# Optimization experiments

Hardware: AMD Instinct MI355X
Metric: run time of the kernel (lower is better)

Reference implementation:

```python
import jax, jax.numpy as jnp
import numpy as np

N, D_IN = 65536, 512
X_DIMS = [512, 2048, 2048, 512]
Y_DIMS = [512, 1024, 512]
T = 2            # n_treatments
OUT_DIM = 1


def setup_inputs() -> dict:
    key = jax.random.key(0)
    ks = iter(jax.random.split(key, 32))
    s = 0.02
    inp = {
        "x": jax.random.normal(next(ks), (N, D_IN), dtype=jnp.float32),
        "treatment": jax.random.randint(next(ks), (N,), 0, T, dtype=jnp.int64),
        # shared trunk MLP (Linear+ReLU after EVERY linear, per original code)
        "Wx0": jax.random.normal(next(ks), (X_DIMS[0], X_DIMS[1]), jnp.float32) * s,
        "bx0": jnp.zeros((X_DIMS[1],), jnp.float32),
        "Wx1": jax.random.normal(next(ks), (X_DIMS[1], X_DIMS[2]), jnp.float32) * s,
        "bx1": jnp.zeros((X_DIMS[2],), jnp.float32),
        "Wx2": jax.random.normal(next(ks), (X_DIMS[2], X_DIMS[3]), jnp.float32) * s,
        "bx2": jnp.zeros((X_DIMS[3],), jnp.float32),
        # per-treatment expert MLPs, stacked on leading T axis
        "Wy0": jax.random.normal(next(ks), (T, Y_DIMS[0], Y_DIMS[1]), jnp.float32) * s,
        "by0": jnp.zeros((T, Y_DIMS[1]), jnp.float32),
        "Wy1": jax.random.normal(next(ks), (T, Y_DIMS[1], Y_DIMS[2]), jnp.float32) * s,
        "by1": jnp.zeros((T, Y_DIMS[2]), jnp.float32),
        # per-treatment output heads
        "Wo": jax.random.normal(next(ks), (T, Y_DIMS[2], OUT_DIM), jnp.float32) * s,
        "bo": jnp.zeros((T, OUT_DIM), jnp.float32),
        # propensity head
        "Wt": jax.random.normal(next(ks), (X_DIMS[3], 1), jnp.float32) * s,
        "bt": jnp.zeros((1,), jnp.float32),
    }
    return inp


def reference(x, treatment, Wx0, bx0, Wx1, bx1, Wx2, bx2,
              Wy0, by0, Wy1, by1, Wo, bo, Wt, bt):
    # shared trunk: ReLU follows every Linear (original MLP applies ReLU after
    # the last layer too, because `i < len(dims)-1` is always true in the loop)
    h = jax.nn.relu(x @ Wx0 + bx0)
    h = jax.nn.relu(h @ Wx1 + bx1)
    x_emb = jax.nn.relu(h @ Wx2 + bx2)            # [N, 512]

    # per-treatment experts computed densely, then gathered by treatment id.
    # This is the dense-equivalent of SplitStreams -> MLP -> GatherStreams:
    # GatherStreams sorts by original row index, so row n of the output is the
    # treatment-`t[n]` head applied to x_emb[n].
    g = jax.nn.relu(jnp.einsum('nd,tdh->nth', x_emb, Wy0) + by0)   # [N,T,1024]
    g = jax.nn.relu(jnp.einsum('nth,thk->ntk', g, Wy1) + by1)      # [N,T,512]
    y_all = jnp.einsum('ntk,tko->nto', g, Wo) + bo                 # [N,T,1]

    t_idx = treatment.astype(jnp.int32).reshape(-1)
    y = jnp.take_along_axis(y_all, t_idx[:, None, None], axis=1)[:, 0, :]  # [N,1]

    # softmax over a size-1 axis -> all ones, but kept faithful to the source
    t_out = jax.nn.softmax(x_emb @ Wt + bt, axis=1)                # [N,1]
    return y, x_emb, t_out
```

## Files before the change

kernel.cpp:

```cpp
#include <hip/hip_runtime.h>
#include <hip/hip_bf16.h>
#include <cstdint>

#define NROWS 65536
#define TTREAT 2

typedef __bf16 bf16x8 __attribute__((ext_vector_type(8)));
typedef float f32x4 __attribute__((ext_vector_type(4)));
typedef unsigned short u16;
typedef u16 u16x8 __attribute__((ext_vector_type(8)));

#define GLOBAL_AS __attribute__((address_space(1)))
#define LDS_AS __attribute__((address_space(3)))

__device__ __forceinline__ int swz_col(int col, int row) {
    return (col & ~63) | (((((col >> 3) & 7) ^ (row & 7)) << 3)) | (col & 7);
}

__device__ __forceinline__ u16 f32_to_bf16_bits(float f) {
    union { float f; uint32_t u; } v; v.f = f;
    uint32_t u = v.u;
    return (u16)((u + 0x7FFFu + ((u >> 16) & 1u)) >> 16);
}

__device__ __forceinline__ float bf16_bits_to_f32(u16 b) {
    union { uint32_t u; float f; } v; v.u = ((uint32_t)b) << 16;
    return v.f;
}

__global__ void cvt_f32_bf16(const float4* __restrict__ src, u16x8* __restrict__ dst, int n8) {
    int i = blockIdx.x * blockDim.x + threadIdx.x;
    if (i >= n8) return;
    float4 a = src[2 * i], b = src[2 * i + 1];
    u16x8 r;
    r[0] = f32_to_bf16_bits(a.x); r[1] = f32_to_bf16_bits(a.y);
    r[2] = f32_to_bf16_bits(a.z); r[3] = f32_to_bf16_bits(a.w);
    r[4] = f32_to_bf16_bits(b.x); r[5] = f32_to_bf16_bits(b.y);
    r[6] = f32_to_bf16_bits(b.z); r[7] = f32_to_bf16_bits(b.w);
    int row = i >> 6;
    int j = (i & ~7) | ((i ^ row) & 7);
    dst[j] = r;
}

__global__ void transpose_w(const float* __restrict__ src, u16* __restrict__ dst, int K, int M) {
    __shared__ float tile[32][33];
    size_t boff = (size_t)blockIdx.z * K * M;
    src += boff; dst += boff;
    int m0 = blockIdx.x * 32, k0 = blockIdx.y * 32;
    int tx = threadIdx.x, ty = threadIdx.y;
#pragma unroll
    for (int i = 0; i < 32; i += 8)
        tile[ty + i][tx] = src[(size_t)(k0 + ty + i) * M + m0 + tx];
    __syncthreads();
#pragma unroll
    for (int i = 0; i < 32; i += 8) {
        int row = m0 + ty + i, col = k0 + tx;
        dst[(size_t)row * K + swz_col(col, row)] = f32_to_bf16_bits(tile[tx][ty + i]);
    }
}

__global__ void zero_cnt(int* cnt) {
    if (threadIdx.x < TTREAT) cnt[threadIdx.x] = 0;
}

__global__ void partition_rows(const int* __restrict__ treat, int* __restrict__ idx, int* __restrict__ cnt) {
    __shared__ int waveCnt1[4];
    __shared__ int blockBase[2];
    const int tid = threadIdx.x;
    const int i = blockIdx.x * 256 + tid;
    const int wave = tid >> 6, lane = tid & 63;
    const int t = treat[i];
    const unsigned long long m1 = __ballot(t == 1);
    const int n1 = __popcll(m1);
    if (lane == 0) waveCnt1[wave] = n1;
    __syncthreads();
    const int w0 = waveCnt1[0], w1 = waveCnt1[1], w2 = waveCnt1[2], w3 = waveCnt1[3];
    const int tot1 = w0 + w1 + w2 + w3;
    if (tid == 0) blockBase[0] = atomicAdd(&cnt[0], 256 - tot1);
    else if (tid == 64) blockBase[1] = atomicAdd(&cnt[1], tot1);
    __syncthreads();
    int waveOff1 = 0;
    if (wave > 0) waveOff1 += w0;
    if (wave > 1) waveOff1 += w1;
    if (wave > 2) waveOff1 += w2;
    const int below1 = (int)__popcll(m1 & ((1ull << lane) - 1ull));
    int pos;
    if (t == 1) pos = blockBase[1] + waveOff1 + below1;
    else        pos = blockBase[0] + (wave * 64 - waveOff1) + (lane - below1);
    idx[t * NROWS + pos] = i;
}

template <bool GATHER, bool WRITE_F32>
__global__ void gemm_bias_relu(const u16* __restrict__ A, const u16* __restrict__ Bt,
                               const float* __restrict__ bias,
                               u16* __restrict__ C, float* __restrict__ C32,
                               const int* __restrict__ idx, const int* __restrict__ cntp,
                               int nrows, int chunkStart, int maxRows, int K, int M) {
    int rows = (cntp ? *cntp : nrows) - chunkStart;
    if (rows > maxRows) rows = maxRows;
    int rowBase = blockIdx.y * 128;
    if (rows <= 0 || rowBase >= rows) return;
    int colBase = blockIdx.x * 128;

    __shared__ __align__(16) u16 As[128 * 64];
    __shared__ __align__(16) u16 Bs[128 * 64];

    const int tid = threadIdx.x;
    const int wave = tid >> 6, lane = tid & 63;
    const int quad = lane >> 4, l16 = lane & 15;
    const int wm = wave >> 1, wn = wave & 1;

    const int r0 = tid >> 3;
    const int kc = (tid & 7) * 8;

    size_t a_off[4], b_off[4];
#pragma unroll
    for (int it = 0; it < 4; ++it) {
        int r = rowBase + r0 + it * 32;
        if (GATHER) {
            int rc = r < rows ? r : (rows - 1);
            int g = idx[rc];
            int kcg = ((((tid & 7) ^ (r & 7) ^ (g & 7)) & 7) * 8);
            a_off[it] = (size_t)g * K + kcg;
        } else {
            a_off[it] = (size_t)r * K + kc;
        }
        int c = colBase + r0 + it * 32;
        b_off[it] = (size_t)c * K + kc;
    }

    f32x4 acc[4][4] = {};

    for (int k0 = 0; k0 < K; k0 += 64) {
        __syncthreads();
#pragma unroll
        for (int it = 0; it < 4; ++it) {
            __builtin_amdgcn_global_load_lds(
                (const GLOBAL_AS void*)(A + a_off[it] + k0),
                (LDS_AS void*)(&As[(it * 256 + wave * 64) * 8]), 16, 0, 0);
            __builtin_amdgcn_global_load_lds(
                (const GLOBAL_AS void*)(Bt + b_off[it] + k0),
                (LDS_AS void*)(&Bs[(it * 256 + wave * 64) * 8]), 16, 0, 0);
        }
        __syncthreads();
#pragma unroll
        for (int kk = 0; kk < 2; ++kk) {
            bf16x8 aF[4], bF[4];
            const int csw = ((kk * 4 + quad) ^ (l16 & 7)) * 8;
#pragma unroll
            for (int mi = 0; mi < 4; ++mi)
                aF[mi] = *(const bf16x8*)&As[(wm * 64 + mi * 16 + l16) * 64 + csw];
#pragma unroll
            for (int ni = 0; ni < 4; ++ni)
                bF[ni] = *(const bf16x8*)&Bs[(wn * 64 + ni * 16 + l16) * 64 + csw];
#pragma unroll
            for (int mi = 0; mi < 4; ++mi)
#pragma unroll
                for (int ni = 0; ni < 4; ++ni)
                    acc[mi][ni] = __builtin_amdgcn_mfma_f32_16x16x32_bf16(
                        aF[mi], bF[ni], acc[mi][ni], 0, 0, 0);
        }
    }

    float bv[4];
#pragma unroll
    for (int ni = 0; ni < 4; ++ni) bv[ni] = bias[colBase + wn * 64 + ni * 16 + l16];

#pragma unroll
    for (int mi = 0; mi < 4; ++mi) {
        int rloc = rowBase + wm * 64 + mi * 16 + quad * 4;
#pragma unroll
        for (int ni = 0; ni < 4; ++ni) {
            int col = colBase + wn * 64 + ni * 16 + l16;
#pragma unroll
            for (int r = 0; r < 4; ++r) {
                int row = rloc + r;
                if (row < rows) {
                    float v = acc[mi][ni][r] + bv[ni];
                    v = v > 0.f ? v : 0.f;
                    C[(size_t)row * M + swz_col(col, row)] = f32_to_bf16_bits(v);
                    if (WRITE_F32) C32[(size_t)row * M + col] = v;
                }
            }
        }
    }
}

__global__ void head_kernel(const u16* __restrict__ g2, const int* __restrict__ idx,
                            const int* __restrict__ cntp, int chunkStart, int maxRows,
                            const float* __restrict__ Wo,
                            const float* __restrict__ bo, float* __restrict__ y) {
    int rows = *cntp - chunkStart;
    if (rows > maxRows) rows = maxRows;
    int wave = threadIdx.x >> 6, lane = threadIdx.x & 63;
    int pos = blockIdx.x * 4 + wave;
    if (pos >= rows) return;
    const u16* grow = g2 + (size_t)pos * 512;
    u16x8 gv = *(const u16x8*)&grow[lane * 8];
    int logical = (lane & ~7) | ((lane ^ pos) & 7);
    const float4* w4 = (const float4*)Wo + logical * 2;
    float4 w0 = w4[0], w1 = w4[1];
    float s = 0.f;
    s += bf16_bits_to_f32(gv[0]) * w0.x + bf16_bits_to_f32(gv[1]) * w0.y;
    s += bf16_bits_to_f32(gv[2]) * w0.z + bf16_bits_to_f32(gv[3]) * w0.w;
    s += bf16_bits_to_f32(gv[4]) * w1.x + bf16_bits_to_f32(gv[5]) * w1.y;
    s += bf16_bits_to_f32(gv[6]) * w1.z + bf16_bits_to_f32(gv[7]) * w1.w;
#pragma unroll
    for (int off = 32; off > 0; off >>= 1) s += __shfl_down(s, off);
    if (lane == 0) y[idx[pos]] = s + bo[0];
}

__global__ void ones_kernel(float* __restrict__ dst, int n) {
    int i = blockIdx.x * 256 + threadIdx.x;
    if (i < n) dst[i] = 1.0f;
}

extern "C" void kernel_launch(void* const* d_in, const int* in_sizes, int n_in,
                              void* d_out, int out_size, void* d_ws, size_t ws_size,
                              hipStream_t stream) {
    const float* x   = (const float*)d_in[0];
    const int* treat = (const int*)d_in[1];
    const float* Wx0 = (const float*)d_in[2];
    const float* bx0 = (const float*)d_in[3];
    const float* Wx1 = (const float*)d_in[4];
    const float* bx1 = (const float*)d_in[5];
    const float* Wx2 = (const float*)d_in[6];
    const float* bx2 = (const float*)d_in[7];
    const float* Wy0 = (const float*)d_in[8];
    const float* by0 = (const float*)d_in[9];
    const float* Wy1 = (const float*)d_in[10];
    const float* by1 = (const float*)d_in[11];
    const float* Wo  = (const float*)d_in[12];
    const float* bo  = (const float*)d_in[13];

    float* out_y  = (float*)d_out;
    float* out_xe = out_y + NROWS;
    float* out_t  = out_xe + (size_t)NROWS * 512;

    const size_t FIXED = ((size_t)(2048 * 512 + 2048 * 2048 + 512 * 2048
                          + TTREAT * 1024 * 512 + TTREAT * 512 * 1024
                          + (size_t)NROWS * 512) * 2)
                          + (size_t)TTREAT * NROWS * 4 + (1 << 20);
    int R = 512;
    const int cands[6] = {16384, 8192, 4096, 2048, 1024, 512};
    for (int ci = 0; ci < 6; ++ci) {
        if (FIXED + (size_t)cands[ci] * 12288 <= ws_size) { R = cands[ci]; break; }
    }
    const int NCHUNK = NROWS / R;

    size_t off = 0;
    auto carve = [&](size_t bytes) {
        void* p = (char*)d_ws + off;
        off += (bytes + 255) & ~(size_t)255;
        return p;
    };
    u16* Wx0t = (u16*)carve((size_t)2048 * 512 * 2);
    u16* Wx1t = (u16*)carve((size_t)2048 * 2048 * 2);
    u16* Wx2t = (u16*)carve((size_t)512 * 2048 * 2);
    u16* Wy0t = (u16*)carve((size_t)TTREAT * 1024 * 512 * 2);
    u16* Wy1t = (u16*)carve((size_t)TTREAT * 512 * 1024 * 2);
    u16* xe   = (u16*)carve((size_t)NROWS * 512 * 2);
    int* idx  = (int*)carve((size_t)TTREAT * NROWS * 4);
    int* cnt  = (int*)carve(256);
    u16* xbc  = (u16*)carve((size_t)R * 512 * 2);
    u16* h1c  = (u16*)carve((size_t)R * 2048 * 2);
    u16* h2c  = (u16*)carve((size_t)R * 2048 * 2);
    u16* g1c  = (u16*)carve((size_t)R * 1024 * 2);
    u16* g2c  = (u16*)carve((size_t)R * 512 * 2);

    dim3 tb32(32, 8);

    transpose_w<<<dim3(2048 / 32, 512 / 32, 1), tb32, 0, stream>>>(Wx0, Wx0t, 512, 2048);
    transpose_w<<<dim3(2048 / 32, 2048 / 32, 1), tb32, 0, stream>>>(Wx1, Wx1t, 2048, 2048);
    transpose_w<<<dim3(512 / 32, 2048 / 32, 1), tb32, 0, stream>>>(Wx2, Wx2t, 2048, 512);
    transpose_w<<<dim3(1024 / 32, 512 / 32, TTREAT), tb32, 0, stream>>>(Wy0, Wy0t, 512, 1024);
    transpose_w<<<dim3(512 / 32, 1024 / 32, TTREAT), tb32, 0, stream>>>(Wy1, Wy1t, 1024, 512);

    zero_cnt<<<1, 64, 0, stream>>>(cnt);
    partition_rows<<<NROWS / 256, 256, 0, stream>>>(treat, idx, cnt);

    const int gy = R / 128;

    for (int c = 0; c < NCHUNK; ++c) {
        int cS = c * R;
        cvt_f32_bf16<<<(R * 512 / 8 + 255) / 256, 256, 0, stream>>>(
            (const float4*)(x + (size_t)cS * 512), (u16x8*)xbc, R * 512 / 8);
        gemm_bias_relu<false, false><<<dim3(2048 / 128, gy), 256, 0, stream>>>(
            xbc, Wx0t, bx0, h1c, nullptr, nullptr, nullptr, NROWS, cS, R, 512, 2048);
        gemm_bias_relu<false, false><<<dim3(2048 / 128, gy), 256, 0, stream>>>(
            h1c, Wx1t, bx1, h2c, nullptr, nullptr, nullptr, NROWS, cS, R, 2048, 2048);
        gemm_bias_relu<false, true><<<dim3(512 / 128, gy), 256, 0, stream>>>(
            h2c, Wx2t, bx2, xe + (size_t)cS * 512, out_xe + (size_t)cS * 512,
            nullptr, nullptr, NROWS, cS, R, 2048, 512);
    }

    for (int t = 0; t < TTREAT; ++t) {
        const int* idx_t = idx + (size_t)t * NROWS;
        for (int c = 0; c < NCHUNK; ++c) {
            int cS = c * R;
            gemm_bias_relu<true, false><<<dim3(1024 / 128, gy), 256, 0, stream>>>(
                xe, Wy0t + (size_t)t * 1024 * 512, by0 + (size_t)t * 1024,
                g1c, nullptr, idx_t + cS, cnt + t, NROWS, cS, R, 512, 1024);
            gemm_bias_relu<false, false><<<dim3(512 / 128, gy), 256, 0, stream>>>(
                g1c, Wy1t + (size_t)t * 512 * 1024, by1 + (size_t)t * 512,
                g2c, nullptr, nullptr, cnt + t, NROWS, cS, R, 1024, 512);
            head_kernel<<<R / 4, 256, 0, stream>>>(
                g2c, idx_t + cS, cnt + t, cS, R, Wo + (size_t)t * 512, bo + t, out_y);
        }
    }

    ones_kernel<<<NROWS / 256, 256, 0, stream>>>(out_t, NROWS);
}
```

Baseline: 1.548 ms.

## Fuse output head into second expert GEMM epilogue with atomic accumulation

Removes the separate head kernel and the g2 intermediate buffer. The second expert GEMM's epilogue now computes the dot product with Wo directly from the accumulators and atomically adds partial sums into y, which is pre-initialised with the bias by a new init kernel that also writes the ones output. Dropping g2 shrinks the per-row workspace, and larger chunk sizes (up to all rows) are allowed, which cuts launch count. The costs are atomics (four column blocks per row) and a nondeterministic summation order.

```diff
diff --git a/kernel.cpp b/kernel.cpp
--- a/kernel.cpp
+++ b/kernel.cpp
@@ -21,11 +21,6 @@
     union { float f; uint32_t u; } v; v.f = f;
     uint32_t u = v.u;
     return (u16)((u + 0x7FFFu + ((u >> 16) & 1u)) >> 16);
-}
-
-__device__ __forceinline__ float bf16_bits_to_f32(u16 b) {
-    union { uint32_t u; float f; } v; v.u = ((uint32_t)b) << 16;
-    return v.f;
 }
 
 __global__ void cvt_f32_bf16(const float4* __restrict__ src, u16x8* __restrict__ dst, int n8) {
@@ -90,12 +85,19 @@
     idx[t * NROWS + pos] = i;
 }
 
-template <bool GATHER, bool WRITE_F32>
+__global__ void init_outputs(const int* __restrict__ treat, const float* __restrict__ bo,
+                             float* __restrict__ y, float* __restrict__ t_out) {
+    int i = blockIdx.x * 256 + threadIdx.x;
+    if (i < NROWS) { y[i] = bo[treat[i]]; t_out[i] = 1.0f; }
+}
+
+template <bool GATHER, bool WRITE_F32, bool FUSE_HEAD>
 __global__ void gemm_bias_relu(const u16* __restrict__ A, const u16* __restrict__ Bt,
                                const float* __restrict__ bias,
                                u16* __restrict__ C, float* __restrict__ C32,
                                const int* __restrict__ idx, const int* __restrict__ cntp,
-                               int nrows, int chunkStart, int maxRows, int K, int M) {
+                               int nrows, int chunkStart, int maxRows, int K, int M,
+                               const float* __restrict__ Wo, float* __restrict__ y) {
     int rows = (cntp ? *cntp : nrows) - chunkStart;
     if (rows > maxRows) rows = maxRows;
     int rowBase = blockIdx.y * 128;
@@ -166,53 +168,58 @@
 #pragma unroll
     for (int ni = 0; ni < 4; ++ni) bv[ni] = bias[colBase + wn * 64 + ni * 16 + l16];
 
-#pragma unroll
-    for (int mi = 0; mi < 4; ++mi) {
-        int rloc = rowBase + wm * 64 + mi * 16 + quad * 4;
-#pragma unroll
-        for (int ni = 0; ni < 4; ++ni) {
-            int col = colBase + wn * 64 + ni * 16 + l16;
+    if (FUSE_HEAD) {
+        float wv[4];
+#pragma unroll
+        for (int ni = 0; ni < 4; ++ni) wv[ni] = Wo[colBase + wn * 64 + ni * 16 + l16];
+        float hs[4][4];
+#pragma unroll
+        for (int mi = 0; mi < 4; ++mi)
 #pragma unroll
             for (int r = 0; r < 4; ++r) {
-                int row = rloc + r;
-                if (row < rows) {
+                float s = 0.f;
+#pragma unroll
+                for (int ni = 0; ni < 4; ++ni) {
                     float v = acc[mi][ni][r] + bv[ni];
                     v = v > 0.f ? v : 0.f;
-                    C[(size_t)row * M + swz_col(col, row)] = f32_to_bf16_bits(v);
-                    if (WRITE_F32) C32[(size_t)row * M + col] = v;
+                    s += v * wv[ni];
+                }
+                hs[mi][r] = s;
+            }
+#pragma unroll
+        for (int mi = 0; mi < 4; ++mi)
+#pragma unroll
+            for (int r = 0; r < 4; ++r) {
+                float s = hs[mi][r];
+                s += __shfl_down(s, 8, 16);
+                s += __shfl_down(s, 4, 16);
+                s += __shfl_down(s, 2, 16);
+                s += __shfl_down(s, 1, 16);
+                if (l16 == 0) {
+                    int row = rowBase + wm * 64 + mi * 16 + quad * 4 + r;
+                    if (row < rows) atomicAdd(&y[idx[row]], s);
                 }
             }
-        }
-    }
-}
-
-__global__ void head_kernel(const u16* __restrict__ g2, const int* __restrict__ idx,
-                            const int* __restrict__ cntp, int chunkStart, int maxRows,
-                            const float* __restrict__ Wo,
-                            const float* __restrict__ bo, float* __restrict__ y) {
-    int rows = *cntp - chunkStart;
-    if (rows > maxRows) rows = maxRows;
-    int wave = threadIdx.x >> 6, lane = threadIdx.x & 63;
-    int pos = blockIdx.x * 4 + wave;
-    if (pos >= rows) return;
-    const u16* grow = g2 + (size_t)pos * 512;
-    u16x8 gv = *(const u16x8*)&grow[lane * 8];
-    int logical = (lane & ~7) | ((lane ^ pos) & 7);
-    const float4* w4 = (const float4*)Wo + logical * 2;
-    float4 w0 = w4[0], w1 = w4[1];
-    float s = 0.f;
-    s += bf16_bits_to_f32(gv[0]) * w0.x + bf16_bits_to_f32(gv[1]) * w0.y;
-    s += bf16_bits_to_f32(gv[2]) * w0.z + bf16_bits_to_f32(gv[3]) * w0.w;
-    s += bf16_bits_to_f32(gv[4]) * w1.x + bf16_bits_to_f32(gv[5]) * w1.y;
-    s += bf16_bits_to_f32(gv[6]) * w1.z + bf16_bits_to_f32(gv[7]) * w1.w;
-#pragma unroll
-    for (int off = 32; off > 0; off >>= 1) s += __shfl_down(s, off);
-    if (lane == 0) y[idx[pos]] = s + bo[0];
-}
-
-__global__ void ones_kernel(float* __restrict__ dst, int n) {
-    int i = blockIdx.x * 256 + threadIdx.x;
-    if (i < n) dst[i] = 1.0f;
+    } else {
+#pragma unroll
+        for (int mi = 0; mi < 4; ++mi) {
+            int rloc = rowBase + wm * 64 + mi * 16 + quad * 4;
+#pragma unroll
+            for (int ni = 0; ni < 4; ++ni) {
+                int col = colBase + wn * 64 + ni * 16 + l16;
+#pragma unroll
+                for (int r = 0; r < 4; ++r) {
+                    int row = rloc + r;
+                    if (row < rows) {
+                        float v = acc[mi][ni][r] + bv[ni];
+                        v = v > 0.f ? v : 0.f;
+                        C[(size_t)row * M + swz_col(col, row)] = f32_to_bf16_bits(v);
+                        if (WRITE_F32) C32[(size_t)row * M + col] = v;
+                    }
+                }
+            }
+        }
+    }
 }
 
 extern "C" void kernel_launch(void* const* d_in, const int* in_sizes, int n_in,
@@ -242,9 +249,9 @@
                           + (size_t)NROWS * 512) * 2)
                           + (size_t)TTREAT * NROWS * 4 + (1 << 20);
     int R = 512;
-    const int cands[6] = {16384, 8192, 4096, 2048, 1024, 512};
-    for (int ci = 0; ci < 6; ++ci) {
-        if (FIXED + (size_t)cands[ci] * 12288 <= ws_size) { R = cands[ci]; break; }
+    const int cands[8] = {65536, 32768, 16384, 8192, 4096, 2048, 1024, 512};
+    for (int ci = 0; ci < 8; ++ci) {
+        if (FIXED + (size_t)cands[ci] * 11264 <= ws_size) { R = cands[ci]; break; }
     }
     const int NCHUNK = NROWS / R;
 
@@ -266,7 +273,6 @@
     u16* h1c  = (u16*)carve((size_t)R * 2048 * 2);
     u16* h2c  = (u16*)carve((size_t)R * 2048 * 2);
     u16* g1c  = (u16*)carve((size_t)R * 1024 * 2);
-    u16* g2c  = (u16*)carve((size_t)R * 512 * 2);
 
     dim3 tb32(32, 8);
 
@@ -279,35 +285,37 @@
     zero_cnt<<<1, 64, 0, stream>>>(cnt);
     partition_rows<<<NROWS / 256, 256, 0, stream>>>(treat, idx, cnt);
 
+    init_outputs<<<NROWS / 256, 256, 0, stream>>>(treat, bo, out_y, out_t);
+
     const int gy = R / 128;
 
     for (int c = 0; c < NCHUNK; ++c) {
         int cS = c * R;
         cvt_f32_bf16<<<(R * 512 / 8 + 255) / 256, 256, 0, stream>>>(
             (const float4*)(x + (size_t)cS * 512), (u16x8*)xbc, R * 512 / 8);
-        gemm_bias_relu<false, false><<<dim3(2048 / 128, gy), 256, 0, stream>>>(
-            xbc, Wx0t, bx0, h1c, nullptr, nullptr, nullptr, NROWS, cS, R, 512, 2048);
-        gemm_bias_relu<false, false><<<dim3(2048 / 128, gy), 256, 0, stream>>>(
-            h1c, Wx1t, bx1, h2c, nullptr, nullptr, nullptr, NROWS, cS, R, 2048, 2048);
-        gemm_bias_relu<false, true><<<dim3(512 / 128, gy), 256, 0, stream>>>(
+        gemm_bias_relu<false, false, false><<<dim3(2048 / 128, gy), 256, 0, stream>>>(
+            xbc, Wx0t, bx0, h1c, nullptr, nullptr, nullptr, NROWS, cS, R, 512, 2048,
+            nullptr, nullptr);
+        gemm_bias_relu<false, false, false><<<dim3(2048 / 128, gy), 256, 0, stream>>>(
+            h1c, Wx1t, bx1, h2c, nullptr, nullptr, nullptr, NROWS, cS, R, 2048, 2048,
+            nullptr, nullptr);
+        gemm_bias_relu<false, true, false><<<dim3(512 / 128, gy), 256, 0, stream>>>(
             h2c, Wx2t, bx2, xe + (size_t)cS * 512, out_xe + (size_t)cS * 512,
-            nullptr, nullptr, NROWS, cS, R, 2048, 512);
+            nullptr, nullptr, NROWS, cS, R, 2048, 512, nullptr, nullptr);
     }
 
     for (int t = 0; t < TTREAT; ++t) {
         const int* idx_t = idx + (size_t)t * NROWS;
         for (int c = 0; c < NCHUNK; ++c) {
             int cS = c * R;
-            gemm_bias_relu<true, false><<<dim3(1024 / 128, gy), 256, 0, stream>>>(
+            gemm_bias_relu<true, false, false><<<dim3(1024 / 128, gy), 256, 0, stream>>>(
                 xe, Wy0t + (size_t)t * 1024 * 512, by0 + (size_t)t * 1024,
-                g1c, nullptr, idx_t + cS, cnt + t, NROWS, cS, R, 512, 1024);
-            gemm_bias_relu<false, false><<<dim3(512 / 128, gy), 256, 0, stream>>>(
+                g1c, nullptr, idx_t + cS, cnt + t, NROWS, cS, R, 512, 1024,
+                nullptr, nullptr);
+            gemm_bias_relu<false, false, true><<<dim3(512 / 128, gy), 256, 0, stream>>>(
                 g1c, Wy1t + (size_t)t * 512 * 1024, by1 + (size_t)t * 512,
-                g2c, nullptr, nullptr, cnt + t, NROWS, cS, R, 1024, 512);
-            head_kernel<<<R / 4, 256, 0, stream>>>(
-                g2c, idx_t + cS, cnt + t, cS, R, Wo + (size_t)t * 512, bo + t, out_y);
-        }
-    }
-
-    ones_kernel<<<NROWS / 256, 256, 0, stream>>>(out_t, NROWS);
-}
+                nullptr, nullptr, idx_t + cS, cnt + t, NROWS, cS, R, 1024, 512,
+                Wo + (size_t)t * 512, out_y);
+        }
+    }
+}
```

Result: faster. 1.489 ms (-3.8%).
